# Kernel tuning notes

Measured on AMD Instinct MI355X. Metric: run time of the kernel, lower is better.

The kernel has to match this reference:

```python
import jax, jax.numpy as jnp
import numpy as np
from jax import lax


def setup_inputs() -> dict:
    key = jax.random.key(0)
    kx, kk = jax.random.split(key)
    B, H, W, Cin, Cout, K = 32, 128, 128, 128, 128, 3
    X = jax.random.normal(kx, (B, H, W, Cin), dtype=jnp.float32)
    kernel = jax.random.normal(kk, (B, K, K, Cin, Cout), dtype=jnp.float32)
    return {"X": X, "kernel": kernel}


def reference(X, kernel):
    """Per-sample dynamic conv2d: each batch element gets its own HWIO kernel.

    Equivalent math to the TF depthwise-trick + reduce_sum, but expressed as a
    vmapped standard convolution (fuses the input-channel reduction, avoiding
    the huge [H',W',B*Cin,Cout] intermediate). Padding = 'VALID'.
    """
    dn = ('NHWC', 'HWIO', 'NHWC')

    def conv_one(x, k):
        # x: [H, W, Cin], k: [kh, kw, Cin, Cout] -> [H', W', Cout]
        return lax.conv_general_dilated(
            x[None], k, window_strides=(1, 1), padding='VALID',
            dimension_numbers=dn)[0]

    return jax.vmap(conv_one)(X, kernel)  # [B, H', W', Cout]
```

## Files before the change

### kernel.cpp

```cpp
#include <hip/hip_runtime.h>
#include <stdint.h>

typedef __attribute__((ext_vector_type(8))) short bf16x8;
typedef __attribute__((ext_vector_type(4))) float f32x4;
typedef __attribute__((ext_vector_type(4))) unsigned short u16x4;

#define NB 32
#define HH 128
#define WW 128
#define CI 128
#define CO 128
#define HO 126
#define WO 126
#define TH 16
#define TW 16
#define PHh 18
#define PWw 18
#define NROW (PHh * PWw)
#define RSTR 72
#define RSTRB 144

__device__ __forceinline__ unsigned short f2bf(float f) {
  union { float f; unsigned u; } x; x.f = f;
  unsigned u = x.u;
  u += 0x7FFFu + ((u >> 16) & 1u);
  return (unsigned short)(u >> 16);
}

__device__ __forceinline__ unsigned cvtpk_bf16(float a, float b) {
  unsigned r;
  asm("v_cvt_pk_bf16_f32 %0, %1, %2" : "=v"(r) : "v"(a), "v"(b));
  return r;
}

__global__ void prep_kt(const float* __restrict__ kin, unsigned short* __restrict__ ktr) {
  __shared__ unsigned short t[CI * CO];
  int bp = blockIdx.x;
  int b = bp / 9, p = bp % 9;
  const float* src = kin + (size_t)bp * (CI * CO);
  unsigned short* dstb = ktr + (size_t)b * (9 * CI * CO);
  for (int i = threadIdx.x; i < CI * CO / 4; i += blockDim.x) {
    f32x4 v = *(const f32x4*)(src + i * 4);
    u16x4 o;
    o.x = f2bf(v.x); o.y = f2bf(v.y); o.z = f2bf(v.z); o.w = f2bf(v.w);
    *(u16x4*)&t[i * 4] = o;
  }
  __syncthreads();
  for (int j = threadIdx.x; j < 2048; j += blockDim.x) {
    int lane = j & 63, f = (j >> 6) & 7, sl = j >> 9;
    int ch = sl >> 1, kc = sl & 1;
    int co = (f >> 2) * 64 + (f & 3) * 16 + (lane & 15);
    int ci0 = ch * 64 + kc * 32 + (lane >> 4) * 8;
    bf16x8 v;
#pragma unroll
    for (int e = 0; e < 8; ++e) v[e] = t[(ci0 + e) * CO + co];
    int slice = (ch * 9 + p) * 2 + kc;
    *(bf16x8*)&dstb[(size_t)slice * 4096 + f * 512 + lane * 8] = v;
  }
}

__global__ void conv_naive(const float* __restrict__ X, const float* __restrict__ Kf,
                           float* __restrict__ out) {
  int idx = blockIdx.x * blockDim.x + threadIdx.x;
  if (idx >= NB * HO * WO * CO) return;
  int co = idx & 127, t = idx >> 7;
  int wp = t % WO; t /= WO;
  int hp = t % HO; int b = t / HO;
  const float* xb = X + (size_t)b * HH * WW * CI;
  const float* kb = Kf + (size_t)b * 9 * CI * CO;
  float s = 0.f;
  for (int p = 0; p < 9; ++p) {
    int kh = p / 3, kw = p % 3;
    const float* xr = xb + ((size_t)(hp + kh) * WW + (wp + kw)) * CI;
    const float* kr = kb + (size_t)p * CI * CO + co;
    for (int ci = 0; ci < CI; ++ci) s += xr[ci] * kr[(size_t)ci * CO];
  }
  out[idx] = s;
}

__global__ __launch_bounds__(512, 4) void conv_main(
    const float* __restrict__ X, const unsigned short* __restrict__ Kt,
    float* __restrict__ out) {
  __shared__ unsigned short lds_a[NROW * RSTR];

  const int tid = threadIdx.x;
  const int lane = tid & 63;
  const int wid = tid >> 6;
  const int wr = wid >> 1, wc = wid & 1;

  const int l = blockIdx.x;
  const int xcd = l & 7, j = l >> 3;
  const int b = xcd * 4 + (j >> 6);
  const int t = j & 63;
  const int ht = t >> 3, wt = t & 7;
  const int h0 = ht * TH, w0 = wt * TW;
  const int ks = lane >> 4, lr = lane & 15;

  const float* xb = X + (size_t)b * HH * WW * CI;

  const int ci4 = tid & 15;
  const int row0 = tid >> 4;
  const int hi0 = (row0 >= PWw) ? 1 : 0;
  const int wi0 = row0 - hi0 * PWw;
  char* const dst0 = (char*)lds_a + row0 * RSTRB + ci4 * 8;

  auto stageA = [&](int ch) {
    int h = hi0, w = wi0;
    const float* srcb = xb + ch * 64 + ci4 * 4;
#pragma unroll
    for (int k = 0; k < 11; ++k) {
      if (k < 10 || tid < 64) {
        int gh = h0 + h, gw = w0 + w;
        bool ok = (gh | gw) < HH;
        const float* src = srcb + ((size_t)(((gh & 127) << 7) + (gw & 127)) << 7);
        f32x4 v = *(const f32x4*)src;
        uint2 o;
        o.x = ok ? cvtpk_bf16(v.x, v.y) : 0u;
        o.y = ok ? cvtpk_bf16(v.z, v.w) : 0u;
        *(uint2*)(dst0 + k * (32 * RSTRB)) = o;
      }
      w += 14;
      int wrap = (w >= PWw) ? 1 : 0;
      h += 1 + wrap;
      w -= wrap ? PWw : 0;
    }
  };

  const int aoff = ((wr * 4) * PWw + lr) * RSTRB + ks * 16;
  const char* ldsb = (const char*)lds_a;

  f32x4 zero = {0.f, 0.f, 0.f, 0.f};
  f32x4 acc[4][4];
#pragma unroll
  for (int m = 0; m < 4; ++m)
#pragma unroll
    for (int n = 0; n < 4; ++n) acc[m][n] = zero;

  const unsigned short* ktw = Kt + (size_t)b * 9 * CI * CO + (wc * 4) * 512 + lane * 8;

  bf16x8 Hf[4];
  auto loadBh = [&](int slice) {
#pragma unroll
    for (int n = 0; n < 4; ++n)
      Hf[n] = *(const bf16x8*)&ktw[(size_t)slice * 4096 + n * 512];
  };

#pragma unroll 1
  for (int ch = 0; ch < 2; ++ch) {
    if (ch) __syncthreads();
    loadBh(ch * 18);
    stageA(ch);
    __syncthreads();

#pragma unroll
    for (int kh = 0; kh < 3; ++kh) {
#pragma unroll
      for (int jj = 0; jj < 6; ++jj) {
        const int kw = jj >> 1, kc = jj & 1;
        const int s = kh * 6 + jj;
        bf16x8 af[4];
#pragma unroll
        for (int m = 0; m < 4; ++m)
          af[m] = *(const bf16x8*)(ldsb + aoff +
                                   ((m + kh) * PWw * RSTRB + kw * RSTRB + kc * 64));
        __builtin_amdgcn_s_setprio(1);
#pragma unroll
        for (int m = 0; m < 4; ++m)
#pragma unroll
          for (int n = 0; n < 4; ++n)
            acc[m][n] = __builtin_amdgcn_mfma_f32_16x16x32_bf16(af[m], Hf[n], acc[m][n], 0, 0, 0);
        __builtin_amdgcn_s_setprio(0);
        if (s < 17) loadBh(ch * 18 + s + 1);
      }
    }
  }

  float* ob = out + (size_t)b * HO * WO * CO;
#pragma unroll
  for (int m = 0; m < 4; ++m) {
    int hp = h0 + wr * 4 + m;
    if (hp >= HO) continue;
#pragma unroll
    for (int r = 0; r < 4; ++r) {
      int wp = w0 + ks * 4 + r;
      if (wp >= WO) continue;
#pragma unroll
      for (int n = 0; n < 4; ++n) {
        int co = wc * 64 + n * 16 + lr;
        ob[((size_t)hp * WO + wp) * CO + co] = acc[m][n][r];
      }
    }
  }
}

extern "C" void kernel_launch(void* const* d_in, const int* in_sizes, int n_in,
                              void* d_out, int out_size, void* d_ws, size_t ws_size,
                              hipStream_t stream) {
  const float* X = (const float*)d_in[0];
  const float* Kf = (const float*)d_in[1];
  float* out = (float*)d_out;
  size_t need = (size_t)NB * 9 * CI * CO * sizeof(unsigned short);
  if (d_ws != nullptr && ws_size >= need) {
    unsigned short* ktr = (unsigned short*)d_ws;
    prep_kt<<<dim3(NB * 9), 256, 0, stream>>>(Kf, ktr);
    conv_main<<<dim3(2048), 512, 0, stream>>>(X, ktr, out);
  } else {
    int total = NB * HO * WO * CO;
    conv_naive<<<(total + 255) / 256, 256, 0, stream>>>(X, Kf, out);
  }
}
```

Before: 204.3 us.

## Switch conv main loop to 32x32x16 MFMA with triple-buffered B fragments

Replaces the 16x16x32 bf16 MFMA tiling with 32x32x16 MFMA, where each wave computes 2x2 tiles of 32 pixels by 32 output channels. The kernel pre-layout in prep_kt is reworked to match the new B fragment layout. B loads move to a three-deep register ring prefetched two steps ahead, including across the channel-chunk boundary. Launch bounds drop to 3 waves per SIMD to make room for the registers. The larger MFMA needs fewer A/B fragment loads per FLOP, at the cost of higher register pressure and lower occupancy.

```diff
diff --git a/kernel.cpp b/kernel.cpp
--- a/kernel.cpp
+++ b/kernel.cpp
@@ -2,6 +2,7 @@
 #include <stdint.h>
 
 typedef __attribute__((ext_vector_type(8))) short bf16x8;
+typedef __attribute__((ext_vector_type(16))) float f32x16;
 typedef __attribute__((ext_vector_type(4))) float f32x4;
 typedef __attribute__((ext_vector_type(4))) unsigned short u16x4;
 
@@ -46,16 +47,15 @@
     *(u16x4*)&t[i * 4] = o;
   }
   __syncthreads();
-  for (int j = threadIdx.x; j < 2048; j += blockDim.x) {
-    int lane = j & 63, f = (j >> 6) & 7, sl = j >> 9;
-    int ch = sl >> 1, kc = sl & 1;
-    int co = (f >> 2) * 64 + (f & 3) * 16 + (lane & 15);
-    int ci0 = ch * 64 + kc * 32 + (lane >> 4) * 8;
+  for (int u = threadIdx.x; u < 2048; u += blockDim.x) {
+    int kgg = u >> 8;
+    int j = u & 255;
+    int co = j >> 1, ci8 = (j & 1) * 8;
     bf16x8 v;
 #pragma unroll
-    for (int e = 0; e < 8; ++e) v[e] = t[(ci0 + e) * CO + co];
-    int slice = (ch * 9 + p) * 2 + kc;
-    *(bf16x8*)&dstb[(size_t)slice * 4096 + f * 512 + lane * 8] = v;
+    for (int e = 0; e < 8; ++e) v[e] = t[(kgg * 16 + ci8 + e) * CO + co];
+    int sl = (kgg >> 2) * 36 + p * 4 + (kgg & 3);
+    *(bf16x8*)&dstb[(size_t)sl * 2048 + co * 16 + ci8] = v;
   }
 }
 
@@ -78,7 +78,7 @@
   out[idx] = s;
 }
 
-__global__ __launch_bounds__(512, 4) void conv_main(
+__global__ __launch_bounds__(512, 3) void conv_main(
     const float* __restrict__ X, const unsigned short* __restrict__ Kt,
     float* __restrict__ out) {
   __shared__ unsigned short lds_a[NROW * RSTR];
@@ -94,7 +94,6 @@
   const int t = j & 63;
   const int ht = t >> 3, wt = t & 7;
   const int h0 = ht * TH, w0 = wt * TW;
-  const int ks = lane >> 4, lr = lane & 15;
 
   const float* xb = X + (size_t)b * HH * WW * CI;
 
@@ -126,68 +125,74 @@
     }
   };
 
-  const int aoff = ((wr * 4) * PWw + lr) * RSTRB + ks * 16;
-  const char* ldsb = (const char*)lds_a;
-
-  f32x4 zero = {0.f, 0.f, 0.f, 0.f};
-  f32x4 acc[4][4];
-#pragma unroll
-  for (int m = 0; m < 4; ++m)
-#pragma unroll
-    for (int n = 0; n < 4; ++n) acc[m][n] = zero;
-
-  const unsigned short* ktw = Kt + (size_t)b * 9 * CI * CO + (wc * 4) * 512 + lane * 8;
-
-  bf16x8 Hf[4];
-  auto loadBh = [&](int slice) {
-#pragma unroll
-    for (int n = 0; n < 4; ++n)
-      Hf[n] = *(const bf16x8*)&ktw[(size_t)slice * 4096 + n * 512];
+  const int hsub = (lane >> 4) & 1, wl = lane & 15, kk = lane >> 5;
+  const int abase = ((wr * 4 + hsub) * PWw + wl) * RSTR + kk * 8;
+
+  const unsigned short* ktb = Kt + (size_t)b * (9 * CI * CO) +
+                              (wc * 2) * 512 + (lane & 31) * 16 + kk * 8;
+  bf16x8 Hf[3][2];
+  auto loadB = [&](bf16x8 (&dst)[2], int sl) {
+    dst[0] = *(const bf16x8*)(ktb + (size_t)sl * 2048);
+    dst[1] = *(const bf16x8*)(ktb + (size_t)sl * 2048 + 512);
   };
+
+  f32x16 zero16 = {0.f, 0.f, 0.f, 0.f, 0.f, 0.f, 0.f, 0.f,
+                   0.f, 0.f, 0.f, 0.f, 0.f, 0.f, 0.f, 0.f};
+  f32x16 acc[2][2];
+#pragma unroll
+  for (int mt = 0; mt < 2; ++mt)
+#pragma unroll
+    for (int g = 0; g < 2; ++g) acc[mt][g] = zero16;
 
 #pragma unroll 1
   for (int ch = 0; ch < 2; ++ch) {
     if (ch) __syncthreads();
-    loadBh(ch * 18);
+    loadB(Hf[0], ch * 36);
+    loadB(Hf[1], ch * 36 + 1);
     stageA(ch);
     __syncthreads();
 
 #pragma unroll
     for (int kh = 0; kh < 3; ++kh) {
 #pragma unroll
-      for (int jj = 0; jj < 6; ++jj) {
-        const int kw = jj >> 1, kc = jj & 1;
-        const int s = kh * 6 + jj;
-        bf16x8 af[4];
-#pragma unroll
-        for (int m = 0; m < 4; ++m)
-          af[m] = *(const bf16x8*)(ldsb + aoff +
-                                   ((m + kh) * PWw * RSTRB + kw * RSTRB + kc * 64));
-        __builtin_amdgcn_s_setprio(1);
-#pragma unroll
-        for (int m = 0; m < 4; ++m)
-#pragma unroll
-          for (int n = 0; n < 4; ++n)
-            acc[m][n] = __builtin_amdgcn_mfma_f32_16x16x32_bf16(af[m], Hf[n], acc[m][n], 0, 0, 0);
-        __builtin_amdgcn_s_setprio(0);
-        if (s < 17) loadBh(ch * 18 + s + 1);
+      for (int kw = 0; kw < 3; ++kw) {
+#pragma unroll
+        for (int kg = 0; kg < 4; ++kg) {
+          const int r = kh * 12 + kw * 4 + kg;
+          if (r < 34) loadB(Hf[(r + 2) % 3], ch * 36 + r + 2);
+          else if (ch == 0) loadB(Hf[(r + 2) % 3], 36 + (r - 34));
+          bf16x8 af[2];
+#pragma unroll
+          for (int mt = 0; mt < 2; ++mt)
+            af[mt] = *(const bf16x8*)&lds_a[abase +
+                     (((mt * 2 + kh) * PWw + kw) * RSTR + kg * 16)];
+          __builtin_amdgcn_s_setprio(1);
+#pragma unroll
+          for (int mt = 0; mt < 2; ++mt)
+#pragma unroll
+            for (int g = 0; g < 2; ++g)
+              acc[mt][g] = __builtin_amdgcn_mfma_f32_32x32x16_bf16(
+                  af[mt], Hf[r % 3][g], acc[mt][g], 0, 0, 0);
+          __builtin_amdgcn_s_setprio(0);
+        }
       }
     }
   }
 
   float* ob = out + (size_t)b * HO * WO * CO;
-#pragma unroll
-  for (int m = 0; m < 4; ++m) {
-    int hp = h0 + wr * 4 + m;
-    if (hp >= HO) continue;
-#pragma unroll
-    for (int r = 0; r < 4; ++r) {
-      int wp = w0 + ks * 4 + r;
-      if (wp >= WO) continue;
-#pragma unroll
-      for (int n = 0; n < 4; ++n) {
-        int co = wc * 64 + n * 16 + lr;
-        ob[((size_t)hp * WO + wp) * CO + co] = acc[m][n][r];
+  const int co0 = wc * 64 + (lane & 31);
+#pragma unroll
+  for (int mt = 0; mt < 2; ++mt) {
+#pragma unroll
+    for (int g = 0; g < 2; ++g) {
+      const int co = co0 + g * 32;
+#pragma unroll
+      for (int reg = 0; reg < 16; ++reg) {
+        const int M = (reg & 3) + 8 * (reg >> 2) + 4 * kk;
+        const int hp = h0 + wr * 4 + mt * 2 + (M >> 4);
+        const int wp = w0 + (M & 15);
+        if (hp < HO && wp < WO)
+          ob[((size_t)hp * WO + wp) * CO + co] = acc[mt][g][reg];
       }
     }
   }
```

After: 247.3 us. 1.21x slower.
